# Performance work log

Measured on AMD Instinct MI355X. Metric: run time of the kernel, lower is better.

## Reference

```python
import jax, jax.numpy as jnp
import numpy as np

NUM_HEADS = 64
HEAD_DIM = 8

def setup_inputs() -> dict:
    key = jax.random.key(0)
    k1, k2, k3, k4, k5 = jax.random.split(key, 5)
    s = 0.02
    return {
        'x': jax.random.normal(k1, (4, 8192, 2048), dtype=jnp.float32),
        'w_qkv': jax.random.normal(k2, (768, 2048), dtype=jnp.float32) * s,
        'w_z': jax.random.normal(k3, (512, 2048), dtype=jnp.float32) * s,
        'w_b': jax.random.normal(k4, (64, 2048), dtype=jnp.float32) * s,
        'w_a': jax.random.normal(k5, (64, 2048), dtype=jnp.float32) * s,
    }

def reference(x, w_qkv, w_z, w_b, w_a):
    B, S, _ = x.shape
    qkv = jnp.einsum('bsh,dh->bsd', x, w_qkv)                     # [B,S,768]
    z = jnp.einsum('bsh,dh->bsd', x, w_z)                          # [B,S,512]
    z = z.reshape(B, S, NUM_HEADS, HEAD_DIM)
    b = jax.nn.sigmoid(jnp.einsum('bsh,dh->bsd', x, w_b))          # [B,S,64]
    a = jnp.einsum('bsh,dh->bsd', x, w_a) * b                      # [B,S,64]
    out = (qkv.sum(-1, keepdims=True)
           + z.sum(-1).sum(-1, keepdims=True)
           + a.sum(-1, keepdims=True))                             # [B,S,1]
    return out
```

## Files before the change

kernel.cpp:

```cpp
#include <hip/hip_runtime.h>
#include <stdint.h>

using bf16x8_t = __attribute__((ext_vector_type(8))) __bf16;
using f32x4_t  = __attribute__((ext_vector_type(4))) float;
using u16x8_t  = __attribute__((ext_vector_type(8))) unsigned short;

#define KD 2048

static __device__ __forceinline__ unsigned short f2bf(float f) {
  union { float f; unsigned u; } v; v.f = f;
  unsigned r = v.u + 0x7fffu + ((v.u >> 16) & 1u);
  return (unsigned short)(r >> 16);
}

__global__ void k_prep(const float* __restrict__ wqkv, const float* __restrict__ wz,
                       const float* __restrict__ wb, const float* __restrict__ wa,
                       float* __restrict__ wsum, unsigned short* __restrict__ wbf3) {
  __shared__ float red[4][8];
  const int b = blockIdx.x, t = threadIdx.x;
  if (b < 128) {
    const int u = b * 256 + t;
    const int l = u & 63;
    const int vv = u >> 6;
    const int nf = vv & 7;
    const int s  = vv >> 3;
    const int k  = s * 32 + ((l >> 4) << 3);
    const int c  = nf * 16 + (l & 15);
    const float* src = (c < 64) ? (wa + (size_t)c * KD + k)
                                : (wb + (size_t)(c - 64) * KD + k);
    f32x4_t v0 = *(const f32x4_t*)(src);
    f32x4_t v1 = *(const f32x4_t*)(src + 4);
    u16x8_t o;
    o[0]=f2bf(v0[0]); o[1]=f2bf(v0[1]); o[2]=f2bf(v0[2]); o[3]=f2bf(v0[3]);
    o[4]=f2bf(v1[0]); o[5]=f2bf(v1[1]); o[6]=f2bf(v1[2]); o[7]=f2bf(v1[3]);
    *(u16x8_t*)(wbf3 + (size_t)u * 8) = o;
  } else {
    const int bw = b - 128;
    const int c = t & 7;
    const int rg = t >> 3;
    const int h = bw * 8 + c;
    float s = 0.f;
    #pragma unroll 8
    for (int i = 0; i < 40; ++i) {
      const int r = rg + 32 * i;
      const float* p = (r < 768) ? (wqkv + (size_t)r * KD)
                                 : (wz + (size_t)(r - 768) * KD);
      s += p[h];
    }
    s += __shfl_xor(s, 8, 64);
    s += __shfl_xor(s, 16, 64);
    s += __shfl_xor(s, 32, 64);
    const int lane = t & 63, wv = t >> 6;
    if (lane < 8) red[wv][lane] = s;
    __syncthreads();
    if (t < 8) wsum[bw * 8 + t] = red[0][t] + red[1][t] + red[2][t] + red[3][t];
  }
}

__global__ __launch_bounds__(256, 3) void k_main(
    const float* __restrict__ x, const unsigned short* __restrict__ wbf3,
    const float* __restrict__ wsum, float* __restrict__ out)
{
  __shared__ __align__(16) unsigned char lds[49152];
  float* swb = (float*)(lds + 40960);
  const int t = threadIdx.x;
  const int lane = t & 63;
  const int wv = t >> 6;
  const int g = lane >> 4;
  const int r15 = lane & 15;
  const size_t tile = (size_t)blockIdx.x * 64;

  {
    f32x4_t a = *(const f32x4_t*)(wsum + t * 8);
    f32x4_t b = *(const f32x4_t*)(wsum + t * 8 + 4);
    *(f32x4_t*)(swb + t * 8) = a;
    *(f32x4_t*)(swb + t * 8 + 4) = b;
  }
  __syncthreads();

  f32x4_t acc[8];
  #pragma unroll
  for (int i = 0; i < 8; ++i) acc[i] = f32x4_t{0.f, 0.f, 0.f, 0.f};
  float s0 = 0.f;

  auto STAGE_W = [&](int it) {
    unsigned char* wbp = lds + 24576 + (it & 1) * 8192;
    const unsigned short* gw = wbf3 + (size_t)it * 4096 + lane * 8;
    #pragma unroll
    for (int i = 0; i < 2; ++i) {
      const int ch = wv * 2 + i;
      __builtin_amdgcn_global_load_lds(
          (const __attribute__((address_space(1))) void*)(gw + ch * 512),
          (__attribute__((address_space(3))) void*)(wbp + ch * 1024), 16, 0, 0);
    }
  };
  auto STAGE_X = [&](int it, int bsel) {
    unsigned char* xbp = lds + bsel * 8192;
    #pragma unroll
    for (int i = 0; i < 2; ++i) {
      const int ch = wv * 2 + i;
      const int r = ch * 8 + (lane >> 3);
      const int c = (lane & 7) ^ (r & 7);
      const float* src = x + (tile + r) * KD + it * 32 + c * 4;
      __builtin_amdgcn_global_load_lds(
          (const __attribute__((address_space(1))) void*)src,
          (__attribute__((address_space(3))) void*)(xbp + ch * 1024), 16, 0, 0);
    }
  };
  auto COMPUTE = [&](int it, int xbsel) {
    const unsigned char* xbp = lds + xbsel * 8192;
    const unsigned char* wbp = lds + 24576 + (it & 1) * 8192;
    const float* wsp = swb + it * 32 + g * 8;
    f32x4_t w0 = *(const f32x4_t*)(wsp);
    f32x4_t w1 = *(const f32x4_t*)(wsp + 4);
    const int r = wv * 16 + r15;
    const unsigned char* xr = xbp + r * 128;
    f32x4_t lo = *(const f32x4_t*)(xr + (((g * 2)     ^ (r15 & 7)) * 16));
    f32x4_t hi = *(const f32x4_t*)(xr + (((g * 2 + 1) ^ (r15 & 7)) * 16));
    bf16x8_t af;
    af[0] = (__bf16)lo[0]; af[1] = (__bf16)lo[1];
    af[2] = (__bf16)lo[2]; af[3] = (__bf16)lo[3];
    af[4] = (__bf16)hi[0]; af[5] = (__bf16)hi[1];
    af[6] = (__bf16)hi[2]; af[7] = (__bf16)hi[3];
    s0 += lo[0]*w0[0] + lo[1]*w0[1] + lo[2]*w0[2] + lo[3]*w0[3]
        + hi[0]*w1[0] + hi[1]*w1[1] + hi[2]*w1[2] + hi[3]*w1[3];
    #pragma unroll
    for (int nf = 0; nf < 8; ++nf) {
      bf16x8_t bfr = *(const bf16x8_t*)(wbp + (nf * 64 + lane) * 16);
      acc[nf] = __builtin_amdgcn_mfma_f32_16x16x32_bf16(af, bfr, acc[nf], 0, 0, 0);
    }
  };

  STAGE_W(0);
  STAGE_X(0, 0);
  STAGE_X(1, 1);

  int xb = 0;
  for (int it = 0; it < 63; ++it) {
    asm volatile("s_waitcnt vmcnt(2)" ::: "memory");
    __builtin_amdgcn_s_barrier();
    __builtin_amdgcn_sched_barrier(0);
    STAGE_W(it + 1);
    if (it < 62) {
      int b2 = xb + 2; if (b2 >= 3) b2 -= 3;
      STAGE_X(it + 2, b2);
    }
    COMPUTE(it, xb);
    ++xb; if (xb == 3) xb = 0;
  }
  asm volatile("s_waitcnt vmcnt(0)" ::: "memory");
  __builtin_amdgcn_s_barrier();
  __builtin_amdgcn_sched_barrier(0);
  COMPUTE(63, xb);

  s0 += __shfl_xor(s0, 16, 64);
  s0 += __shfl_xor(s0, 32, 64);

  #pragma unroll
  for (int r = 0; r < 4; ++r) {
    float v = 0.f;
    #pragma unroll
    for (int nf = 0; nf < 4; ++nf) {
      float av = acc[nf][r];
      float bv = acc[nf + 4][r];
      v += av / (1.f + __expf(-bv));
    }
    v += __shfl_xor(v, 1, 64);
    v += __shfl_xor(v, 2, 64);
    v += __shfl_xor(v, 4, 64);
    v += __shfl_xor(v, 8, 64);
    const int row = g * 4 + r;
    float s0r = __shfl(s0, row, 64);
    if (r15 == 0) out[tile + wv * 16 + row] = v + s0r;
  }
}

extern "C" void kernel_launch(void* const* d_in, const int* in_sizes, int n_in,
                              void* d_out, int out_size, void* d_ws, size_t ws_size,
                              hipStream_t stream) {
  const float* x    = (const float*)d_in[0];
  const float* wqkv = (const float*)d_in[1];
  const float* wz   = (const float*)d_in[2];
  const float* wb   = (const float*)d_in[3];
  const float* wa   = (const float*)d_in[4];
  float* out = (float*)d_out;

  float* wsum = (float*)d_ws;
  unsigned short* wbf3 = (unsigned short*)((char*)d_ws + 8192);

  k_prep<<<384, 256, 0, stream>>>(wqkv, wz, wb, wa, wsum, wbf3);
  k_main<<<out_size / 64, 256, 0, stream>>>(x, wbf3, wsum, out);
}
```

Baseline: 58.84 us.

## Enlarge tile to 128 rows and K-step 64 with 512-thread blocks

The main kernel now processes 128 rows per block with 8 waves and a 64-wide K step, so the grid is 256 blocks with one block per CU. Buffering changes to two x buffers, and the bf16 weights are staged in pairs of K-steps along with the wsum vector, which is loaded asynchronously into LDS instead of copied up front. Because each wave stages and reads only its own x rows, the second half-step relies on per-wave vmcnt/lgkmcnt waits instead of a block barrier. The goal is fewer barriers and loop iterations and larger loads in flight per block. The cost is lower occupancy (8 waves per CU instead of 12) and a tail of only 256 blocks.

```diff
diff --git a/kernel.cpp b/kernel.cpp
--- a/kernel.cpp
+++ b/kernel.cpp
@@ -57,101 +57,103 @@
   }
 }
 
-__global__ __launch_bounds__(256, 3) void k_main(
+__global__ __launch_bounds__(512, 1) void k_main(
     const float* __restrict__ x, const unsigned short* __restrict__ wbf3,
     const float* __restrict__ wsum, float* __restrict__ out)
 {
-  __shared__ __align__(16) unsigned char lds[49152];
-  float* swb = (float*)(lds + 40960);
+  __shared__ __align__(16) unsigned char lds[132096];
   const int t = threadIdx.x;
   const int lane = t & 63;
   const int wv = t >> 6;
   const int g = lane >> 4;
   const int r15 = lane & 15;
-  const size_t tile = (size_t)blockIdx.x * 64;
-
-  {
-    f32x4_t a = *(const f32x4_t*)(wsum + t * 8);
-    f32x4_t b = *(const f32x4_t*)(wsum + t * 8 + 4);
-    *(f32x4_t*)(swb + t * 8) = a;
-    *(f32x4_t*)(swb + t * 8 + 4) = b;
-  }
-  __syncthreads();
+  const size_t tile = (size_t)blockIdx.x * 128;
 
   f32x4_t acc[8];
   #pragma unroll
   for (int i = 0; i < 8; ++i) acc[i] = f32x4_t{0.f, 0.f, 0.f, 0.f};
   float s0 = 0.f;
 
-  auto STAGE_W = [&](int it) {
-    unsigned char* wbp = lds + 24576 + (it & 1) * 8192;
-    const unsigned short* gw = wbf3 + (size_t)it * 4096 + lane * 8;
+  auto STAGE_WP = [&](int j) {
+    unsigned char* wbp = lds + 65536 + (j & 1) * 33280;
+    const unsigned short* gw = wbf3 + (size_t)j * 16384 + lane * 8;
     #pragma unroll
-    for (int i = 0; i < 2; ++i) {
-      const int ch = wv * 2 + i;
+    for (int i = 0; i < 4; ++i) {
+      const int ch = wv * 4 + i;
       __builtin_amdgcn_global_load_lds(
           (const __attribute__((address_space(1))) void*)(gw + ch * 512),
           (__attribute__((address_space(3))) void*)(wbp + ch * 1024), 16, 0, 0);
     }
+    const float* gws = wsum + j * 128 + lane;
+    __builtin_amdgcn_global_load_lds(
+        (const __attribute__((address_space(1))) void*)gws,
+        (__attribute__((address_space(3))) void*)(wbp + 32768), 4, 0, 0);
+    __builtin_amdgcn_global_load_lds(
+        (const __attribute__((address_space(1))) void*)(gws + 64),
+        (__attribute__((address_space(3))) void*)(wbp + 32768 + 256), 4, 0, 0);
   };
-  auto STAGE_X = [&](int it, int bsel) {
-    unsigned char* xbp = lds + bsel * 8192;
+  auto STAGE_X = [&](int it) {
+    unsigned char* xbp = lds + (it & 1) * 32768;
     #pragma unroll
-    for (int i = 0; i < 2; ++i) {
-      const int ch = wv * 2 + i;
-      const int r = ch * 8 + (lane >> 3);
-      const int c = (lane & 7) ^ (r & 7);
-      const float* src = x + (tile + r) * KD + it * 32 + c * 4;
+    for (int i = 0; i < 4; ++i) {
+      const int ch = wv * 4 + i;
+      const int r = ch * 4 + (lane >> 4);
+      const int c = (lane & 15) ^ (r & 15);
+      const float* src = x + (tile + r) * KD + it * 64 + c * 4;
       __builtin_amdgcn_global_load_lds(
           (const __attribute__((address_space(1))) void*)src,
           (__attribute__((address_space(3))) void*)(xbp + ch * 1024), 16, 0, 0);
     }
   };
-  auto COMPUTE = [&](int it, int xbsel) {
-    const unsigned char* xbp = lds + xbsel * 8192;
-    const unsigned char* wbp = lds + 24576 + (it & 1) * 8192;
-    const float* wsp = swb + it * 32 + g * 8;
-    f32x4_t w0 = *(const f32x4_t*)(wsp);
-    f32x4_t w1 = *(const f32x4_t*)(wsp + 4);
+  auto COMPUTE = [&](int it) {
+    const unsigned char* xbp = lds + (it & 1) * 32768;
+    const unsigned char* wpb = lds + 65536 + ((it >> 1) & 1) * 33280;
+    const unsigned char* wbp = wpb + (it & 1) * 16384;
+    const float* wsp = (const float*)(wpb + 32768 + (it & 1) * 256);
     const int r = wv * 16 + r15;
-    const unsigned char* xr = xbp + r * 128;
-    f32x4_t lo = *(const f32x4_t*)(xr + (((g * 2)     ^ (r15 & 7)) * 16));
-    f32x4_t hi = *(const f32x4_t*)(xr + (((g * 2 + 1) ^ (r15 & 7)) * 16));
-    bf16x8_t af;
-    af[0] = (__bf16)lo[0]; af[1] = (__bf16)lo[1];
-    af[2] = (__bf16)lo[2]; af[3] = (__bf16)lo[3];
-    af[4] = (__bf16)hi[0]; af[5] = (__bf16)hi[1];
-    af[6] = (__bf16)hi[2]; af[7] = (__bf16)hi[3];
-    s0 += lo[0]*w0[0] + lo[1]*w0[1] + lo[2]*w0[2] + lo[3]*w0[3]
-        + hi[0]*w1[0] + hi[1]*w1[1] + hi[2]*w1[2] + hi[3]*w1[3];
+    const unsigned char* xr = xbp + r * 256;
     #pragma unroll
-    for (int nf = 0; nf < 8; ++nf) {
-      bf16x8_t bfr = *(const bf16x8_t*)(wbp + (nf * 64 + lane) * 16);
-      acc[nf] = __builtin_amdgcn_mfma_f32_16x16x32_bf16(af, bfr, acc[nf], 0, 0, 0);
+    for (int kh = 0; kh < 2; ++kh) {
+      const int c0 = kh * 8 + g * 2;
+      f32x4_t lo = *(const f32x4_t*)(xr + ((c0       ^ r15) * 16));
+      f32x4_t hi = *(const f32x4_t*)(xr + (((c0 + 1) ^ r15) * 16));
+      f32x4_t w0 = *(const f32x4_t*)(wsp + kh * 32 + g * 8);
+      f32x4_t w1 = *(const f32x4_t*)(wsp + kh * 32 + g * 8 + 4);
+      bf16x8_t af;
+      af[0] = (__bf16)lo[0]; af[1] = (__bf16)lo[1];
+      af[2] = (__bf16)lo[2]; af[3] = (__bf16)lo[3];
+      af[4] = (__bf16)hi[0]; af[5] = (__bf16)hi[1];
+      af[6] = (__bf16)hi[2]; af[7] = (__bf16)hi[3];
+      s0 += lo[0]*w0[0] + lo[1]*w0[1] + lo[2]*w0[2] + lo[3]*w0[3]
+          + hi[0]*w1[0] + hi[1]*w1[1] + hi[2]*w1[2] + hi[3]*w1[3];
+      #pragma unroll
+      for (int nf = 0; nf < 8; ++nf) {
+        bf16x8_t bfr = *(const bf16x8_t*)(wbp + ((kh * 8 + nf) * 64 + lane) * 16);
+        acc[nf] = __builtin_amdgcn_mfma_f32_16x16x32_bf16(af, bfr, acc[nf], 0, 0, 0);
+      }
     }
   };
 
-  STAGE_W(0);
-  STAGE_X(0, 0);
-  STAGE_X(1, 1);
+  STAGE_WP(0);
+  STAGE_X(0);
+  STAGE_X(1);
 
-  int xb = 0;
-  for (int it = 0; it < 63; ++it) {
-    asm volatile("s_waitcnt vmcnt(2)" ::: "memory");
+  for (int j = 0; j < 16; ++j) {
+    const int itE = j * 2;
+    asm volatile("s_waitcnt vmcnt(4)" ::: "memory");
     __builtin_amdgcn_s_barrier();
     __builtin_amdgcn_sched_barrier(0);
-    STAGE_W(it + 1);
-    if (it < 62) {
-      int b2 = xb + 2; if (b2 >= 3) b2 -= 3;
-      STAGE_X(it + 2, b2);
-    }
-    COMPUTE(it, xb);
-    ++xb; if (xb == 3) xb = 0;
+    if (j < 15) STAGE_WP(j + 1);
+    COMPUTE(itE);
+    asm volatile("s_waitcnt lgkmcnt(0)" ::: "memory");
+    if (itE + 2 < 32) STAGE_X(itE + 2);
+    if (j < 15) { asm volatile("s_waitcnt vmcnt(10)" ::: "memory"); }
+    else        { asm volatile("s_waitcnt vmcnt(0)"  ::: "memory"); }
+    __builtin_amdgcn_sched_barrier(0);
+    COMPUTE(itE + 1);
+    asm volatile("s_waitcnt lgkmcnt(0)" ::: "memory");
+    if (itE + 3 < 32) STAGE_X(itE + 3);
   }
-  asm volatile("s_waitcnt vmcnt(0)" ::: "memory");
-  __builtin_amdgcn_s_barrier();
-  __builtin_amdgcn_sched_barrier(0);
-  COMPUTE(63, xb);
 
   s0 += __shfl_xor(s0, 16, 64);
   s0 += __shfl_xor(s0, 32, 64);
@@ -189,5 +191,5 @@
   unsigned short* wbf3 = (unsigned short*)((char*)d_ws + 8192);
 
   k_prep<<<384, 256, 0, stream>>>(wqkv, wz, wb, wa, wsum, wbf3);
-  k_main<<<out_size / 64, 256, 0, stream>>>(x, wbf3, wsum, out);
+  k_main<<<out_size / 128, 512, 0, stream>>>(x, wbf3, wsum, out);
 }
```

After: 56.15 us. 1.05x faster.
